# Kernel optimization log

Measured on AMD Instinct MI355X. Metric: run time of the kernel, lower is better.

The kernel has to match this reference:

```python
import jax, jax.numpy as jnp
import numpy as np

C_IN = 128
C_QK = C_IN // 8


def setup_inputs() -> dict:
    key = jax.random.key(0)
    kx, kq, kk, kv = jax.random.split(key, 4)
    x = jax.random.normal(kx, (8, C_IN, 64, 64), dtype=jnp.float32)
    # 1x1 conv weights, stored as (c_out, c_in); fan-in scaled init
    s = 1.0 / np.sqrt(C_IN)
    Wq = jax.random.normal(kq, (C_QK, C_IN), dtype=jnp.float32) * s
    Wk = jax.random.normal(kk, (C_QK, C_IN), dtype=jnp.float32) * s
    Wv = jax.random.normal(kv, (C_IN, C_IN), dtype=jnp.float32) * s
    gamma = jnp.ones((1,), dtype=jnp.float32) * 0.5  # nonzero so residual branch matters
    return {"x": x, "Wq": Wq, "Wk": Wk, "Wv": Wv, "gamma": gamma}


def reference(x, Wq, Wk, Wv, gamma):
    b, c, h, w = x.shape
    xt = rearr = x.reshape(b, c, h * w)            # b c n
    q = jnp.einsum('oc,bcn->bno', Wq, xt)          # b n c//8
    k = jnp.einsum('oc,bcn->bon', Wk, xt)          # b c//8 n
    v = jnp.einsum('oc,bcn->bno', Wv, xt)          # b n c
    energy = jnp.einsum('bno,bom->bnm', q, k)      # b n n (no scale, per source)
    attn = jax.nn.softmax(energy, axis=-1)
    out = jnp.einsum('bnm,bmc->bnc', attn, v)      # b n c
    out = out.transpose(0, 2, 1).reshape(b, c, h, w)
    return x + gamma[0] * out
```

## Files before the change

kernel.cpp:

```cpp
#include <hip/hip_runtime.h>
#include <hip/hip_bf16.h>


typedef __bf16 bf16x8 __attribute__((ext_vector_type(8)));
typedef __bf16 bf16x4 __attribute__((ext_vector_type(4)));
typedef float  f32x16 __attribute__((ext_vector_type(16)));
typedef unsigned int uint32x2 __attribute__((ext_vector_type(2)));

static constexpr int Bb = 8, Cc = 128, Nn = 4096, CQ = 16;

__device__ __forceinline__ f32x16 mfma32(bf16x8 a, bf16x8 b, f32x16 c) {
    return __builtin_amdgcn_mfma_f32_32x32x16_bf16(a, b, c, 0, 0, 0);
}
struct HL { __bf16 h, l; };
__device__ __forceinline__ HL hilo(float f) {
    HL r;
    r.h = (__bf16)f;
    r.l = (__bf16)(f - (float)r.h);
    return r;
}
__device__ __forceinline__ unsigned int pack2bf(float a, float b) {
    union { __bf16 h[2]; unsigned int u; } x;
    x.h[0] = (__bf16)a; x.h[1] = (__bf16)b;
    return x.u;
}

__global__ __launch_bounds__(256) void qkv_kernel(
    const float* __restrict__ x, const float* __restrict__ Wq,
    const float* __restrict__ Wk, const float* __restrict__ Wv,
    __bf16* __restrict__ qw, __bf16* __restrict__ kw, __bf16* __restrict__ vw)
{
    const int b = blockIdx.y, n0 = blockIdx.x * 64, t = threadIdx.x;
    const int wave = t >> 6, lane = t & 63, lr = lane & 31, lq = lane >> 5;

    __shared__ __bf16 xh[64][136], xl[64][136];
    __shared__ __bf16 wqh[32][136], wql[32][136];
    __shared__ __bf16 sc[4][32][40];

    {
        const int n = t & 63, ug = t >> 6;
        #pragma unroll
        for (int i = 0; i < 4; ++i) {
            const int ci0 = (ug * 4 + i) * 8;
            float v[8];
            #pragma unroll
            for (int k = 0; k < 8; ++k)
                v[k] = x[((size_t)(b * Cc + ci0 + k)) * Nn + n0 + n];
            bf16x8 h8, l8;
            #pragma unroll
            for (int k = 0; k < 8; ++k) { HL z = hilo(v[k]); h8[k] = z.h; l8[k] = z.l; }
            *(bf16x8*)&xh[n][ci0] = h8;
            *(bf16x8*)&xl[n][ci0] = l8;
        }
    }
    #pragma unroll
    for (int i = 0; i < 8; ++i) {
        int idx = t + i * 256;
        int o = idx >> 7, ci = idx & 127;
        HL zq = hilo(Wq[idx]);
        wqh[o][ci] = zq.h; wql[o][ci] = zq.l;
        HL zk = hilo(Wk[idx]);
        wqh[16 + o][ci] = zk.h; wql[16 + o][ci] = zk.l;
    }
    __syncthreads();

    if (wave < 2) {
        const int nh = wave;
        f32x16 acc = {};
        #pragma unroll
        for (int ks = 0; ks < 8; ++ks) {
            bf16x8 ah = *(const bf16x8*)&wqh[lr][ks * 16 + lq * 8];
            bf16x8 al = *(const bf16x8*)&wql[lr][ks * 16 + lq * 8];
            bf16x8 bh = *(const bf16x8*)&xh[nh * 32 + lr][ks * 16 + lq * 8];
            bf16x8 bl = *(const bf16x8*)&xl[nh * 32 + lr][ks * 16 + lq * 8];
            acc = mfma32(ah, bh, acc);
            acc = mfma32(al, bh, acc);
            acc = mfma32(ah, bl, acc);
        }
        const int tile = (n0 >> 5) + nh;
        __bf16* qb = qw + (((size_t)b * 128 + tile) << 10);
        __bf16* kb = kw + (((size_t)b * 128 + tile) << 10);
        #pragma unroll
        for (int rg = 0; rg < 4; ++rg) {
            bf16x4 h4, l4;
            #pragma unroll
            for (int j = 0; j < 4; ++j) {
                float v = acc[rg * 4 + j];
                if (rg < 2) v *= 1.44269504089f;
                HL z = hilo(v);
                h4[j] = z.h; l4[j] = z.l;
            }
            const int off = (rg & 1) * 256 + lr * 8 + 4 * lq;
            __bf16* base = (rg < 2) ? qb : kb;
            *(bf16x4*)(base + off) = h4;
            *(bf16x4*)(base + 512 + off) = l4;
        }
    }
    {
        int tl[3][2]; int nt;
        if      (wave == 0) { tl[0][0]=2; tl[0][1]=0; nt=1; }
        else if (wave == 1) { tl[0][0]=2; tl[0][1]=1; nt=1; }
        else if (wave == 2) { tl[0][0]=0; tl[0][1]=0; tl[1][0]=1; tl[1][1]=0; tl[2][0]=3; tl[2][1]=0; nt=3; }
        else                { tl[0][0]=0; tl[0][1]=1; tl[1][0]=1; tl[1][1]=1; tl[2][0]=3; tl[2][1]=1; nt=3; }
        for (int ti = 0; ti < nt; ++ti) {
            const int ct = tl[ti][0], nh = tl[ti][1];
            f32x16 acc = {};
            #pragma unroll
            for (int ks = 0; ks < 8; ++ks) {
                const float* wp = Wv + (ct * 32 + lr) * Cc + ks * 16 + lq * 8;
                float4 w0 = *(const float4*)wp;
                float4 w1 = *(const float4*)(wp + 4);
                bf16x8 a = { (__bf16)w0.x, (__bf16)w0.y, (__bf16)w0.z, (__bf16)w0.w,
                             (__bf16)w1.x, (__bf16)w1.y, (__bf16)w1.z, (__bf16)w1.w };
                bf16x8 bh = *(const bf16x8*)&xh[nh * 32 + lr][ks * 16 + lq * 8];
                acc = mfma32(a, bh, acc);
            }
            #pragma unroll
            for (int r = 0; r < 16; ++r) {
                int crow = (r & 3) + 8 * (r >> 2) + 4 * lq;
                sc[wave][crow][lr] = (__bf16)acc[r];
            }
            const int chunk = (n0 >> 5) + nh;
            __bf16* vb = vw + (((size_t)b * 128 + chunk) << 12) + ct * 1024;
            #pragma unroll
            for (int u = 0; u < 2; ++u) {
                bf16x8 row = *(const bf16x8*)&sc[wave][lr][u * 16 + lq * 8];
                *(bf16x8*)(vb + u * 512 + lane * 8) = row;
            }
        }
    }
}

__global__ __launch_bounds__(512, 4) void attn_kernel(
    const float* __restrict__ x, const __bf16* __restrict__ qw,
    const __bf16* __restrict__ kw, const __bf16* __restrict__ vw,
    const float* __restrict__ gamma, float* __restrict__ out)
{
    const int h = blockIdx.x;
    const int b = h & 7;
    const int qt = h >> 3;
    const int t = threadIdx.x;
    const int wave = t >> 6, lane = t & 63, lr = lane & 31, lq = lane >> 5;
    const int kr = wave & 3, ch = wave >> 2;

    __shared__ float accbuf[32][129];
    __shared__ float lbuf[32];

    const __bf16* qb = qw + (((size_t)b * 128 + qt) << 10) + lane * 8;
    const bf16x8 qhi = *(const bf16x8*)qb;
    const bf16x8 qlo = *(const bf16x8*)(qb + 512);

    const __bf16* kwb = kw + (((size_t)b * 128) << 10);
    const __bf16* vwb = vw + (((size_t)b * 128) << 12) + ch * 2048;
    const int c0 = kr * 32;

    bf16x8 khi, klo;
    {
        const __bf16* kp = kwb + ((size_t)c0 << 10) + lane * 8;
        khi = *(const bf16x8*)kp;
        klo = *(const bf16x8*)(kp + 512);
    }

    f32x16 acc0 = {}, acc1 = {};
    float l_part = 0.f;

    for (int it = 0; it < 32; ++it) {
        const __bf16* vp = vwb + ((size_t)(c0 + it) << 12) + lane * 8;
        bf16x8 vf0 = *(const bf16x8*)(vp);
        bf16x8 vf1 = *(const bf16x8*)(vp + 512);
        bf16x8 vf2 = *(const bf16x8*)(vp + 1024);
        bf16x8 vf3 = *(const bf16x8*)(vp + 1536);

        bf16x8 nkh, nkl;
        {
            const int nc = c0 + (it < 31 ? it + 1 : it);
            const __bf16* kp = kwb + ((size_t)nc << 10) + lane * 8;
            nkh = *(const bf16x8*)kp;
            nkl = *(const bf16x8*)(kp + 512);
        }

        f32x16 s = {};
        s = mfma32(khi, qhi, s);
        s = mfma32(klo, qhi, s);
        s = mfma32(khi, qlo, s);

        float p[16];
        #pragma unroll
        for (int r = 0; r < 16; ++r) p[r] = __builtin_amdgcn_exp2f(s[r]);
        l_part += ((((p[0] + p[1]) + (p[2] + p[3])) + ((p[4] + p[5]) + (p[6] + p[7])))
                 + (((p[8] + p[9]) + (p[10] + p[11])) + ((p[12] + p[13]) + (p[14] + p[15]))));

        unsigned int G00 = pack2bf(p[0],  p[1]),  G01 = pack2bf(p[2],  p[3]);
        unsigned int G10 = pack2bf(p[4],  p[5]),  G11 = pack2bf(p[6],  p[7]);
        unsigned int G20 = pack2bf(p[8],  p[9]),  G21 = pack2bf(p[10], p[11]);
        unsigned int G30 = pack2bf(p[12], p[13]), G31 = pack2bf(p[14], p[15]);

        {
            uint32x2 r;
            r = __builtin_amdgcn_permlane32_swap(G00, G10, false, false);
            G00 = r[0]; G10 = r[1];
            r = __builtin_amdgcn_permlane32_swap(G01, G11, false, false);
            G01 = r[0]; G11 = r[1];
            r = __builtin_amdgcn_permlane32_swap(G20, G30, false, false);
            G20 = r[0]; G30 = r[1];
            r = __builtin_amdgcn_permlane32_swap(G21, G31, false, false);
            G21 = r[0]; G31 = r[1];
        }

        union U8 { unsigned int u[4]; bf16x8 v; };
        U8 F0, F1;
        F0.u[0] = G00; F0.u[1] = G01; F0.u[2] = G10; F0.u[3] = G11;
        F1.u[0] = G20; F1.u[1] = G21; F1.u[2] = G30; F1.u[3] = G31;

        acc0 = mfma32(vf0, F0.v, acc0);
        acc0 = mfma32(vf1, F1.v, acc0);
        acc1 = mfma32(vf2, F0.v, acc1);
        acc1 = mfma32(vf3, F1.v, acc1);

        khi = nkh; klo = nkl;
    }

    l_part += __shfl_xor(l_part, 32);

    if (kr == 0) {
        #pragma unroll
        for (int r = 0; r < 16; ++r) {
            int c = ch * 64 + (r & 3) + 8 * (r >> 2) + 4 * lq;
            accbuf[lr][c] = acc0[r];
            accbuf[lr][c + 32] = acc1[r];
        }
        if (wave == 0 && lane < 32) lbuf[lr] = l_part;
    }
    __syncthreads();
    if (kr != 0) {
        #pragma unroll
        for (int r = 0; r < 16; ++r) {
            int c = ch * 64 + (r & 3) + 8 * (r >> 2) + 4 * lq;
            atomicAdd(&accbuf[lr][c], acc0[r]);
            atomicAdd(&accbuf[lr][c + 32], acc1[r]);
        }
        if (ch == 0 && lane < 32) atomicAdd(&lbuf[lr], l_part);
    }
    __syncthreads();

    const float g = gamma[0];
    const int q = t & 31, cg = t >> 5;
    const float linv = 1.0f / lbuf[q];
    const int n0b = qt * 32;
    #pragma unroll
    for (int i = 0; i < 8; ++i) {
        int c = cg + 16 * i;
        size_t idx = ((size_t)(b * Cc + c)) * Nn + n0b + q;
        out[idx] = x[idx] + g * accbuf[q][c] * linv;
    }
}

extern "C" void kernel_launch(void* const* d_in, const int* in_sizes, int n_in,
                              void* d_out, int out_size, void* d_ws, size_t ws_size,
                              hipStream_t stream) {
    const float* x  = (const float*)d_in[0];
    const float* Wq = (const float*)d_in[1];
    const float* Wk = (const float*)d_in[2];
    const float* Wv = (const float*)d_in[3];
    const float* gm = (const float*)d_in[4];

    __bf16* qw = (__bf16*)d_ws;
    __bf16* kw = qw + (size_t)Bb * 128 * 1024;
    __bf16* vw = kw + (size_t)Bb * 128 * 1024;

    qkv_kernel<<<dim3(Nn / 64, Bb), 256, 0, stream>>>(x, Wq, Wk, Wv, qw, kw, vw);
    attn_kernel<<<dim3(Nn / 32 * Bb), 512, 0, stream>>>(x, qw, kw, vw, gm,
                                                        (float*)d_out);
}
```

Baseline: 202.9 us.

## Shrink QKV blocks to 32 columns and software-pipeline K/V loads in attention

The QKV projection kernel now processes 32 spatial positions per block instead of 64, doubling the grid. It also drops the shared-memory staging of Wq/Wk and converts the weights to hi/lo bf16 directly from global memory inside the single wave that computes Q/K. In the attention kernel, the V fragments are now prefetched one iteration ahead together with K, using a peeled final iteration, so global-load latency can overlap the MFMA work. The cost is more registers held live for the prefetched V data and redundant weight reads per block in the projection kernel.

```diff
diff --git a/kernel.cpp b/kernel.cpp
--- a/kernel.cpp
+++ b/kernel.cpp
@@ -25,59 +25,61 @@
     return x.u;
 }
 
-__global__ __launch_bounds__(256) void qkv_kernel(
+__global__ __launch_bounds__(256, 4) void qkv_kernel(
     const float* __restrict__ x, const float* __restrict__ Wq,
     const float* __restrict__ Wk, const float* __restrict__ Wv,
     __bf16* __restrict__ qw, __bf16* __restrict__ kw, __bf16* __restrict__ vw)
 {
-    const int b = blockIdx.y, n0 = blockIdx.x * 64, t = threadIdx.x;
+    const int b = blockIdx.y, tile = blockIdx.x, n0 = tile * 32, t = threadIdx.x;
     const int wave = t >> 6, lane = t & 63, lr = lane & 31, lq = lane >> 5;
 
-    __shared__ __bf16 xh[64][136], xl[64][136];
-    __shared__ __bf16 wqh[32][136], wql[32][136];
-    __shared__ __bf16 sc[4][32][40];
+    __shared__ __bf16 xh[32][136], xl[32][136];
+    __shared__ __bf16 sc[3][32][40];
 
     {
-        const int n = t & 63, ug = t >> 6;
-        #pragma unroll
-        for (int i = 0; i < 4; ++i) {
-            const int ci0 = (ug * 4 + i) * 8;
-            float v[8];
-            #pragma unroll
-            for (int k = 0; k < 8; ++k)
-                v[k] = x[((size_t)(b * Cc + ci0 + k)) * Nn + n0 + n];
-            bf16x8 h8, l8;
-            #pragma unroll
-            for (int k = 0; k < 8; ++k) { HL z = hilo(v[k]); h8[k] = z.h; l8[k] = z.l; }
-            *(bf16x8*)&xh[n][ci0] = h8;
-            *(bf16x8*)&xl[n][ci0] = l8;
-        }
-    }
-    #pragma unroll
-    for (int i = 0; i < 8; ++i) {
-        int idx = t + i * 256;
-        int o = idx >> 7, ci = idx & 127;
-        HL zq = hilo(Wq[idx]);
-        wqh[o][ci] = zq.h; wql[o][ci] = zq.l;
-        HL zk = hilo(Wk[idx]);
-        wqh[16 + o][ci] = zk.h; wql[16 + o][ci] = zk.l;
+        const int n = t & 31, ci0 = (t >> 5) * 16;
+        float v[16];
+        #pragma unroll
+        for (int k = 0; k < 16; ++k)
+            v[k] = x[((size_t)(b * Cc + ci0 + k)) * Nn + n0 + n];
+        bf16x8 h8[2], l8[2];
+        #pragma unroll
+        for (int k = 0; k < 16; ++k) {
+            HL z = hilo(v[k]);
+            h8[k >> 3][k & 7] = z.h;
+            l8[k >> 3][k & 7] = z.l;
+        }
+        *(bf16x8*)&xh[n][ci0]     = h8[0];
+        *(bf16x8*)&xh[n][ci0 + 8] = h8[1];
+        *(bf16x8*)&xl[n][ci0]     = l8[0];
+        *(bf16x8*)&xl[n][ci0 + 8] = l8[1];
     }
     __syncthreads();
 
-    if (wave < 2) {
-        const int nh = wave;
+    if (wave == 0) {
+        const float* wrow = (lr < 16) ? (Wq + (size_t)lr * Cc)
+                                      : (Wk + (size_t)(lr - 16) * Cc);
         f32x16 acc = {};
         #pragma unroll
         for (int ks = 0; ks < 8; ++ks) {
-            bf16x8 ah = *(const bf16x8*)&wqh[lr][ks * 16 + lq * 8];
-            bf16x8 al = *(const bf16x8*)&wql[lr][ks * 16 + lq * 8];
-            bf16x8 bh = *(const bf16x8*)&xh[nh * 32 + lr][ks * 16 + lq * 8];
-            bf16x8 bl = *(const bf16x8*)&xl[nh * 32 + lr][ks * 16 + lq * 8];
+            float4 w0 = *(const float4*)(wrow + ks * 16 + lq * 8);
+            float4 w1 = *(const float4*)(wrow + ks * 16 + lq * 8 + 4);
+            bf16x8 ah, al;
+            HL z;
+            z = hilo(w0.x); ah[0] = z.h; al[0] = z.l;
+            z = hilo(w0.y); ah[1] = z.h; al[1] = z.l;
+            z = hilo(w0.z); ah[2] = z.h; al[2] = z.l;
+            z = hilo(w0.w); ah[3] = z.h; al[3] = z.l;
+            z = hilo(w1.x); ah[4] = z.h; al[4] = z.l;
+            z = hilo(w1.y); ah[5] = z.h; al[5] = z.l;
+            z = hilo(w1.z); ah[6] = z.h; al[6] = z.l;
+            z = hilo(w1.w); ah[7] = z.h; al[7] = z.l;
+            bf16x8 bh = *(const bf16x8*)&xh[lr][ks * 16 + lq * 8];
+            bf16x8 bl = *(const bf16x8*)&xl[lr][ks * 16 + lq * 8];
             acc = mfma32(ah, bh, acc);
             acc = mfma32(al, bh, acc);
             acc = mfma32(ah, bl, acc);
         }
-        const int tile = (n0 >> 5) + nh;
         __bf16* qb = qw + (((size_t)b * 128 + tile) << 10);
         __bf16* kb = kw + (((size_t)b * 128 + tile) << 10);
         #pragma unroll
@@ -95,36 +97,33 @@
             *(bf16x4*)(base + off) = h4;
             *(bf16x4*)(base + 512 + off) = l4;
         }
-    }
-    {
-        int tl[3][2]; int nt;
-        if      (wave == 0) { tl[0][0]=2; tl[0][1]=0; nt=1; }
-        else if (wave == 1) { tl[0][0]=2; tl[0][1]=1; nt=1; }
-        else if (wave == 2) { tl[0][0]=0; tl[0][1]=0; tl[1][0]=1; tl[1][1]=0; tl[2][0]=3; tl[2][1]=0; nt=3; }
-        else                { tl[0][0]=0; tl[0][1]=1; tl[1][0]=1; tl[1][1]=1; tl[2][0]=3; tl[2][1]=1; nt=3; }
+    } else {
+        int cts[2]; int nt;
+        if      (wave == 1) { cts[0] = 0; cts[1] = 1; nt = 2; }
+        else if (wave == 2) { cts[0] = 2; nt = 1; }
+        else                { cts[0] = 3; nt = 1; }
         for (int ti = 0; ti < nt; ++ti) {
-            const int ct = tl[ti][0], nh = tl[ti][1];
+            const int ct = cts[ti];
             f32x16 acc = {};
             #pragma unroll
             for (int ks = 0; ks < 8; ++ks) {
-                const float* wp = Wv + (ct * 32 + lr) * Cc + ks * 16 + lq * 8;
+                const float* wp = Wv + (size_t)(ct * 32 + lr) * Cc + ks * 16 + lq * 8;
                 float4 w0 = *(const float4*)wp;
                 float4 w1 = *(const float4*)(wp + 4);
                 bf16x8 a = { (__bf16)w0.x, (__bf16)w0.y, (__bf16)w0.z, (__bf16)w0.w,
                              (__bf16)w1.x, (__bf16)w1.y, (__bf16)w1.z, (__bf16)w1.w };
-                bf16x8 bh = *(const bf16x8*)&xh[nh * 32 + lr][ks * 16 + lq * 8];
+                bf16x8 bh = *(const bf16x8*)&xh[lr][ks * 16 + lq * 8];
                 acc = mfma32(a, bh, acc);
             }
             #pragma unroll
             for (int r = 0; r < 16; ++r) {
                 int crow = (r & 3) + 8 * (r >> 2) + 4 * lq;
-                sc[wave][crow][lr] = (__bf16)acc[r];
-            }
-            const int chunk = (n0 >> 5) + nh;
-            __bf16* vb = vw + (((size_t)b * 128 + chunk) << 12) + ct * 1024;
+                sc[wave - 1][crow][lr] = (__bf16)acc[r];
+            }
+            __bf16* vb = vw + (((size_t)b * 128 + tile) << 12) + ct * 1024;
             #pragma unroll
             for (int u = 0; u < 2; ++u) {
-                bf16x8 row = *(const bf16x8*)&sc[wave][lr][u * 16 + lq * 8];
+                bf16x8 row = *(const bf16x8*)&sc[wave - 1][lr][u * 16 + lq * 8];
                 *(bf16x8*)(vb + u * 512 + lane * 8) = row;
             }
         }
@@ -150,39 +149,23 @@
     const bf16x8 qhi = *(const bf16x8*)qb;
     const bf16x8 qlo = *(const bf16x8*)(qb + 512);
 
-    const __bf16* kwb = kw + (((size_t)b * 128) << 10);
-    const __bf16* vwb = vw + (((size_t)b * 128) << 12) + ch * 2048;
     const int c0 = kr * 32;
-
-    bf16x8 khi, klo;
-    {
-        const __bf16* kp = kwb + ((size_t)c0 << 10) + lane * 8;
-        khi = *(const bf16x8*)kp;
-        klo = *(const bf16x8*)(kp + 512);
-    }
+    const __bf16* kp = kw + (((size_t)b * 128 + c0) << 10) + lane * 8;
+    const __bf16* vp = vw + (((size_t)b * 128 + c0) << 12) + ch * 2048 + lane * 8;
 
     f32x16 acc0 = {}, acc1 = {};
     float l_part = 0.f;
 
-    for (int it = 0; it < 32; ++it) {
-        const __bf16* vp = vwb + ((size_t)(c0 + it) << 12) + lane * 8;
-        bf16x8 vf0 = *(const bf16x8*)(vp);
-        bf16x8 vf1 = *(const bf16x8*)(vp + 512);
-        bf16x8 vf2 = *(const bf16x8*)(vp + 1024);
-        bf16x8 vf3 = *(const bf16x8*)(vp + 1536);
-
-        bf16x8 nkh, nkl;
-        {
-            const int nc = c0 + (it < 31 ? it + 1 : it);
-            const __bf16* kp = kwb + ((size_t)nc << 10) + lane * 8;
-            nkh = *(const bf16x8*)kp;
-            nkl = *(const bf16x8*)(kp + 512);
-        }
-
+    bf16x8 kh = *(const bf16x8*)kp,          kl = *(const bf16x8*)(kp + 512);
+    bf16x8 v0 = *(const bf16x8*)vp,          v1 = *(const bf16x8*)(vp + 512);
+    bf16x8 v2 = *(const bf16x8*)(vp + 1024), v3 = *(const bf16x8*)(vp + 1536);
+
+    auto body = [&](bf16x8 Kh, bf16x8 Kl, bf16x8 V0, bf16x8 V1,
+                    bf16x8 V2, bf16x8 V3) {
         f32x16 s = {};
-        s = mfma32(khi, qhi, s);
-        s = mfma32(klo, qhi, s);
-        s = mfma32(khi, qlo, s);
+        s = mfma32(Kh, qhi, s);
+        s = mfma32(Kl, qhi, s);
+        s = mfma32(Kh, qlo, s);
 
         float p[16];
         #pragma unroll
@@ -212,13 +195,21 @@
         F0.u[0] = G00; F0.u[1] = G01; F0.u[2] = G10; F0.u[3] = G11;
         F1.u[0] = G20; F1.u[1] = G21; F1.u[2] = G30; F1.u[3] = G31;
 
-        acc0 = mfma32(vf0, F0.v, acc0);
-        acc0 = mfma32(vf1, F1.v, acc0);
-        acc1 = mfma32(vf2, F0.v, acc1);
-        acc1 = mfma32(vf3, F1.v, acc1);
-
-        khi = nkh; klo = nkl;
-    }
+        acc0 = mfma32(V0, F0.v, acc0);
+        acc0 = mfma32(V1, F1.v, acc0);
+        acc1 = mfma32(V2, F0.v, acc1);
+        acc1 = mfma32(V3, F1.v, acc1);
+    };
+
+    for (int it = 0; it < 31; ++it) {
+        kp += 1024; vp += 4096;
+        bf16x8 nkh = *(const bf16x8*)kp,          nkl = *(const bf16x8*)(kp + 512);
+        bf16x8 nv0 = *(const bf16x8*)vp,          nv1 = *(const bf16x8*)(vp + 512);
+        bf16x8 nv2 = *(const bf16x8*)(vp + 1024), nv3 = *(const bf16x8*)(vp + 1536);
+        body(kh, kl, v0, v1, v2, v3);
+        kh = nkh; kl = nkl; v0 = nv0; v1 = nv1; v2 = nv2; v3 = nv3;
+    }
+    body(kh, kl, v0, v1, v2, v3);
 
     l_part += __shfl_xor(l_part, 32);
 
@@ -268,7 +259,7 @@
     __bf16* kw = qw + (size_t)Bb * 128 * 1024;
     __bf16* vw = kw + (size_t)Bb * 128 * 1024;
 
-    qkv_kernel<<<dim3(Nn / 64, Bb), 256, 0, stream>>>(x, Wq, Wk, Wv, qw, kw, vw);
+    qkv_kernel<<<dim3(Nn / 32, Bb), 256, 0, stream>>>(x, Wq, Wk, Wv, qw, kw, vw);
     attn_kernel<<<dim3(Nn / 32 * Bb), 512, 0, stream>>>(x, qw, kw, vw, gm,
                                                         (float*)d_out);
 }
```

New measurement: 191.3 us. -5.7%, faster.
